# Performance work log

Measured on AMD Instinct MI355X. Metric: run time of the kernel, lower is better.

The kernel has to match this reference:

```python
import jax, jax.numpy as jnp
import numpy as np

N = 150000      # active voxels
C = 64          # head input channels
KK = 9          # 3x3 kernel offsets
H = W = 700     # BEV feature map
BN_EPS = 1e-5
HEADS = [("heatmap", 3), ("center", 2), ("center_z", 1), ("dim", 3), ("rot", 2)]


def _build_neighbor_table(seed=0):
    """Submanifold 3x3 neighbor indices for N active voxels on an HxW grid.
    Entry -1 means the neighbor site is inactive (contributes zero)."""
    rng = np.random.default_rng(seed)
    flat = rng.choice(H * W, size=N, replace=False)
    ys, xs = flat // W, flat % W
    lut = np.full(H * W, -1, np.int64)
    lut[flat] = np.arange(N)
    nbr = np.full((N, KK), -1, np.int64)
    k = 0
    for dy in (-1, 0, 1):
        for dx in (-1, 0, 1):
            ny, nx = ys + dy, xs + dx
            valid = (ny >= 0) & (ny < H) & (nx >= 0) & (nx < W)
            nf = np.where(valid, ny * W + nx, 0)
            nbr[:, k] = np.where(valid, lut[nf], -1)
            k += 1
    return nbr


def setup_inputs() -> dict:
    key = jax.random.key(0)
    ks = jax.random.split(key, 2 + 2 * len(HEADS))
    inp = {
        "features": jax.random.normal(ks[0], (N, C), jnp.float32),
        "nbr_idx": jnp.asarray(_build_neighbor_table(), jnp.int32),
        # one 3x3 subm conv per head, stacked: [n_heads, 9, C_in, C_out]
        "W3": jax.random.normal(ks[1], (len(HEADS), KK, C, C), jnp.float32) * 0.05,
        "gamma": jnp.ones((len(HEADS), C), jnp.float32),
        "beta": jnp.zeros((len(HEADS), C), jnp.float32),
    }
    for i, (name, oc) in enumerate(HEADS):
        inp[f"W1_{name}"] = jax.random.normal(ks[2 + i], (C, oc), jnp.float32) * 0.001
        if name == "heatmap":
            inp[f"b1_{name}"] = jnp.full((oc,), -float(np.log((1 - 0.01) / 0.01)), jnp.float32)
        else:
            inp[f"b1_{name}"] = jnp.zeros((oc,), jnp.float32)
    return inp


def _forward(features, nbr_idx, W3, gamma, beta, W1s, b1s):
    valid = nbr_idx >= 0                                  # [N, 9]
    idx = jnp.where(valid, nbr_idx, 0)
    # gather active-neighbor features; missing neighbors -> zero (subm conv)
    gathered = features[idx] * valid[..., None].astype(features.dtype)  # [N, 9, C]
    # all heads share the same input sparse tensor -> batched gather-GEMM
    h = jnp.einsum('nkc,hkco->hno', gathered, W3)         # [n_heads, N, C]
    # BatchNorm1d (training-mode batch stats, biased var) + ReLU
    mean = h.mean(axis=1, keepdims=True)
    var = ((h - mean) ** 2).mean(axis=1, keepdims=True)
    hn = (h - mean) * jax.lax.rsqrt(var + BN_EPS)
    hn = jax.nn.relu(hn * gamma[:, None, :] + beta[:, None, :])
    # per-head 1x1 subm conv == linear on active features
    return tuple(hn[i] @ W1s[i] + b1s[i] for i in range(len(HEADS)))


def reference(features, nbr_idx, W3, gamma, beta,
              W1_heatmap, b1_heatmap, W1_center, b1_center,
              W1_center_z, b1_center_z, W1_dim, b1_dim, W1_rot, b1_rot):
    W1s = [W1_heatmap, W1_center, W1_center_z, W1_dim, W1_rot]
    b1s = [b1_heatmap, b1_center, b1_center_z, b1_dim, b1_rot]
    return _forward(features, nbr_idx, W3, gamma, beta, W1s, b1s)
```

## Files before the change

kernel.cpp:

```cpp
#include <hip/hip_runtime.h>

#define NVOX 150000
#define BM 128
#define MTILES 1172
#define SROW 150016
#define NCOL 320

typedef __attribute__((ext_vector_type(8))) short bf16x8;
typedef __attribute__((ext_vector_type(4))) float f32x4;

__device__ __forceinline__ unsigned short f2bf(float f) {
    unsigned u = __builtin_bit_cast(unsigned, f);
    u += 0x7fffu + ((u >> 16) & 1u);
    return (unsigned short)(u >> 16);
}

__device__ __forceinline__ void gld16(const void* g, void* l) {
    __builtin_amdgcn_global_load_lds(
        (const __attribute__((address_space(1))) unsigned int*)g,
        (__attribute__((address_space(3))) unsigned int*)l, 16, 0, 0);
}

__global__ void prep_feat(const float* __restrict__ src, unsigned short* __restrict__ dst) {
    int i = blockIdx.x * 256 + threadIdx.x;
    if (i < NVOX * 8) {
        const float* s = src + (size_t)i * 8;
        float4 a = *(const float4*)s;
        float4 b = *(const float4*)(s + 4);
        union { bf16x8 v; unsigned short u[8]; } r;
        r.u[0] = f2bf(a.x); r.u[1] = f2bf(a.y); r.u[2] = f2bf(a.z); r.u[3] = f2bf(a.w);
        r.u[4] = f2bf(b.x); r.u[5] = f2bf(b.y); r.u[6] = f2bf(b.z); r.u[7] = f2bf(b.w);
        *(bf16x8*)(dst + (size_t)i * 8) = r.v;
    } else if (i < NVOX * 8 + 8) {
        bf16x8 z = {0, 0, 0, 0, 0, 0, 0, 0};
        *(bf16x8*)(dst + (size_t)i * 8) = z;
    }
}

__global__ void prep_w3(const float* __restrict__ w3, unsigned short* __restrict__ bt,
                        float* __restrict__ stats) {
    int i = blockIdx.x * 256 + threadIdx.x;
    int h = i / 36864;
    int rem = i - h * 36864;
    int kk = rem >> 12;
    int c = (rem >> 6) & 63;
    int o = rem & 63;
    bt[(size_t)(((h * 9 + kk) * 8) + (c >> 3)) * 512 + o * 8 + (c & 7)] = f2bf(w3[i]);
    if (i < 2 * NCOL) stats[i] = 0.f;
}

__global__ __launch_bounds__(256, 4)
void gemm_kernel(const unsigned short* __restrict__ featB,
                 const unsigned short* __restrict__ Bt2,
                 const int* __restrict__ nbr,
                 unsigned short* __restrict__ hbuf,
                 float* __restrict__ stats) {
    __shared__ __align__(16) char smem[37376];
    constexpr int IDX_OFF = 32768;
    constexpr int SRED_OFF = 32768;

    int bid = blockIdx.x;
    int r = bid & 7, q = bid >> 3;
    int ntile = q % 5;
    int mtile = (q / 5) * 8 + r;
    if (mtile >= MTILES) return;
    int m0 = mtile * BM;
    int n0 = ntile * 64;

    int tid = threadIdx.x;
    int w = tid >> 6, lane = tid & 63;
    int quad = lane >> 4, m16 = lane & 15;

    for (int lin = tid; lin < BM * 9; lin += 256) {
        int row = lin / 9, kkq = lin - row * 9;
        int v = -1;
        if (m0 + row < NVOX) v = nbr[(size_t)(m0 + row) * 9 + kkq];
        *(int*)(smem + IDX_OFF + (kkq * BM + row) * 4) = ((v < 0) ? NVOX : v) * 128;
    }
    __syncthreads();

    f32x4 acc[4][2];
#pragma unroll
    for (int mt = 0; mt < 4; ++mt)
#pragma unroll
        for (int nt = 0; nt < 2; ++nt)
            acc[mt][nt] = (f32x4){0.f, 0.f, 0.f, 0.f};

    const char* fb = (const char*)featB;
    const char* bsrc = (const char*)Bt2 + (size_t)ntile * 73728;
    char* sAb[2] = {smem, smem + 16384};

    int mrow = (w >> 1) * 64;
    int ncol = (w & 1) * 32;
    int c16a = w * 2, c16b = w * 2 + 1;
    const char* bb = bsrc + quad * 1024 + (ncol + m16) * 16;

    bf16x8 bfr[2][2][2];

    auto stageA = [&](char* sA, int off0, int off1) {
        gld16(fb + off0 + c16a * 16, sA + c16a * 2048);
        gld16(fb + off1 + c16a * 16, sA + c16a * 2048 + 1024);
        gld16(fb + off0 + c16b * 16, sA + c16b * 2048);
        gld16(fb + off1 + c16b * 16, sA + c16b * 2048 + 1024);
    };

    {
        int o0 = *(const int*)(smem + IDX_OFF + lane * 4);
        int o1 = *(const int*)(smem + IDX_OFF + (64 + lane) * 4);
        bfr[0][0][0] = *(const bf16x8*)(bb);
        bfr[0][0][1] = *(const bf16x8*)(bb + 256);
        bfr[0][1][0] = *(const bf16x8*)(bb + 4096);
        bfr[0][1][1] = *(const bf16x8*)(bb + 4352);
        stageA(sAb[0], o0, o1);
    }

#pragma unroll
    for (int kk = 0; kk < 9; ++kk) {
        const int p = kk & 1;
        if (kk < 8) {
            int o0 = *(const int*)(smem + IDX_OFF + ((kk + 1) * BM + lane) * 4);
            int o1 = *(const int*)(smem + IDX_OFF + ((kk + 1) * BM + 64 + lane) * 4);
            const char* bk = bb + (size_t)(kk + 1) * 8192;
            bfr[p ^ 1][0][0] = *(const bf16x8*)(bk);
            bfr[p ^ 1][0][1] = *(const bf16x8*)(bk + 256);
            bfr[p ^ 1][1][0] = *(const bf16x8*)(bk + 4096);
            bfr[p ^ 1][1][1] = *(const bf16x8*)(bk + 4352);
            stageA(sAb[p ^ 1], o0, o1);
            asm volatile("s_waitcnt vmcnt(8)" ::: "memory");
        } else {
            asm volatile("s_waitcnt vmcnt(0)" ::: "memory");
        }
        asm volatile("s_barrier" ::: "memory");
        __builtin_amdgcn_sched_barrier(0);
        __builtin_amdgcn_s_setprio(1);
#pragma unroll
        for (int ks = 0; ks < 2; ++ks) {
            bf16x8 af[4];
#pragma unroll
            for (int mt = 0; mt < 4; ++mt)
                af[mt] = *(const bf16x8*)(sAb[p] + (ks * 4 + quad) * 2048 +
                                          (mrow + mt * 16 + m16) * 16);
#pragma unroll
            for (int mt = 0; mt < 4; ++mt)
#pragma unroll
                for (int nt = 0; nt < 2; ++nt)
                    acc[mt][nt] = __builtin_amdgcn_mfma_f32_16x16x32_bf16(
                        af[mt], bfr[p][ks][nt], acc[mt][nt], 0, 0, 0);
        }
        __builtin_amdgcn_s_setprio(0);
        __builtin_amdgcn_sched_barrier(0);
        asm volatile("s_barrier" ::: "memory");
    }

#pragma unroll
    for (int mt = 0; mt < 4; ++mt) {
#pragma unroll
        for (int nt = 0; nt < 2; ++nt) {
            int col = ncol + nt * 16 + m16;
            int row = mrow + mt * 16 + quad * 4;
            f32x4 v = acc[mt][nt];
            unsigned lo = (unsigned)f2bf(v.x) | ((unsigned)f2bf(v.y) << 16);
            unsigned hi = (unsigned)f2bf(v.z) | ((unsigned)f2bf(v.w) << 16);
            uint2 pk; pk.x = lo; pk.y = hi;
            *(uint2*)(smem + col * 272 + row * 2) = pk;
        }
    }
    __syncthreads();
#pragma unroll
    for (int it = 0; it < 8; ++it) {
        int col = it * 8 + (tid >> 5);
        int l32 = tid & 31;
        uint2 v = *(const uint2*)(smem + col * 272 + l32 * 8);
        *(uint2*)(hbuf + (size_t)(n0 + col) * SROW + m0 + l32 * 4) = v;
    }

    float s[2], ss[2];
#pragma unroll
    for (int nt = 0; nt < 2; ++nt) {
        float a = 0.f, b = 0.f;
#pragma unroll
        for (int mt = 0; mt < 4; ++mt) {
            f32x4 v = acc[mt][nt];
            a += v.x + v.y + v.z + v.w;
            b += v.x * v.x + v.y * v.y + v.z * v.z + v.w * v.w;
        }
        s[nt] = a; ss[nt] = b;
        s[nt] += __shfl_xor(s[nt], 16); s[nt] += __shfl_xor(s[nt], 32);
        ss[nt] += __shfl_xor(ss[nt], 16); ss[nt] += __shfl_xor(ss[nt], 32);
    }
    if (quad == 0) {
#pragma unroll
        for (int nt = 0; nt < 2; ++nt) {
            float* p = (float*)(smem + SRED_OFF + ((w * 2 + nt) * 16 + m16) * 8);
            p[0] = s[nt]; p[1] = ss[nt];
        }
    }
    __syncthreads();
    if (tid < 64) {
        int col = tid;
        int half = col >> 5, nt = (col >> 4) & 1, mc = col & 15;
        const float* p0 = (const float*)(smem + SRED_OFF + ((half * 2 + nt) * 16 + mc) * 8);
        const float* p1 = (const float*)(smem + SRED_OFF + (((2 + half) * 2 + nt) * 16 + mc) * 8);
        atomicAdd(&stats[n0 + col], p0[0] + p1[0]);
        atomicAdd(&stats[NCOL + n0 + col], p0[1] + p1[1]);
    }
}

__global__ __launch_bounds__(256)
void head_kernel(const unsigned short* __restrict__ hbuf,
                 const float* __restrict__ stats,
                 const float* __restrict__ gamma, const float* __restrict__ beta,
                 const float* __restrict__ W1_0, const float* __restrict__ W1_1,
                 const float* __restrict__ W1_2, const float* __restrict__ W1_3,
                 const float* __restrict__ W1_4,
                 const float* __restrict__ b1_0, const float* __restrict__ b1_1,
                 const float* __restrict__ b1_2, const float* __restrict__ b1_3,
                 const float* __restrict__ b1_4,
                 float* __restrict__ out) {
    __shared__ float sScale[64], sShift[64], sW1[192], sB1[3];
    int h = blockIdx.y;
    const float* W1; const float* b1; int oc; size_t obase;
    if (h == 0)      { W1 = W1_0; b1 = b1_0; oc = 3; obase = 0; }
    else if (h == 1) { W1 = W1_1; b1 = b1_1; oc = 2; obase = 450000; }
    else if (h == 2) { W1 = W1_2; b1 = b1_2; oc = 1; obase = 750000; }
    else if (h == 3) { W1 = W1_3; b1 = b1_3; oc = 3; obase = 900000; }
    else             { W1 = W1_4; b1 = b1_4; oc = 2; obase = 1350000; }

    int tid = threadIdx.x;
    if (tid < 64) {
        int c = h * 64 + tid;
        float mean = stats[c] * (1.f / (float)NVOX);
        float var = stats[NCOL + c] * (1.f / (float)NVOX) - mean * mean;
        float inv = rsqrtf(var + 1e-5f);
        float sc = inv * gamma[c];
        sScale[tid] = sc;
        sShift[tid] = beta[c] - mean * sc;
    }
    for (int i = tid; i < 192; i += 256) {
        int cc = i / 3, jj = i - cc * 3;
        sW1[i] = (jj < oc) ? W1[cc * oc + jj] : 0.f;
    }
    if (tid == 0) {
        sB1[0] = b1[0];
        sB1[1] = (oc >= 2) ? b1[1] : 0.f;
        sB1[2] = (oc >= 3) ? b1[2] : 0.f;
    }
    __syncthreads();

    int n = (blockIdx.x * 256 + tid) * 4;
    if (n >= NVOX) return;
    const unsigned short* hp = hbuf + (size_t)(h * 64) * SROW + n;
    float x[4][3];
#pragma unroll
    for (int rr = 0; rr < 4; ++rr) { x[rr][0] = sB1[0]; x[rr][1] = sB1[1]; x[rr][2] = sB1[2]; }
#pragma unroll 8
    for (int cc = 0; cc < 64; ++cc) {
        uint2 raw = *(const uint2*)(hp + (size_t)cc * SROW);
        float sc = sScale[cc], sh = sShift[cc];
        float w0 = sW1[cc * 3 + 0], w1 = sW1[cc * 3 + 1], w2 = sW1[cc * 3 + 2];
        float v0 = __builtin_bit_cast(float, raw.x << 16);
        float v1 = __builtin_bit_cast(float, raw.x & 0xffff0000u);
        float v2 = __builtin_bit_cast(float, raw.y << 16);
        float v3 = __builtin_bit_cast(float, raw.y & 0xffff0000u);
        v0 = fmaxf(v0 * sc + sh, 0.f); v1 = fmaxf(v1 * sc + sh, 0.f);
        v2 = fmaxf(v2 * sc + sh, 0.f); v3 = fmaxf(v3 * sc + sh, 0.f);
        x[0][0] += v0 * w0; x[0][1] += v0 * w1; x[0][2] += v0 * w2;
        x[1][0] += v1 * w0; x[1][1] += v1 * w1; x[1][2] += v1 * w2;
        x[2][0] += v2 * w0; x[2][1] += v2 * w1; x[2][2] += v2 * w2;
        x[3][0] += v3 * w0; x[3][1] += v3 * w1; x[3][2] += v3 * w2;
    }
#pragma unroll
    for (int rr = 0; rr < 4; ++rr) {
        float* op = out + obase + (size_t)(n + rr) * oc;
        op[0] = x[rr][0];
        if (oc >= 2) op[1] = x[rr][1];
        if (oc >= 3) op[2] = x[rr][2];
    }
}

extern "C" void kernel_launch(void* const* d_in, const int* in_sizes, int n_in,
                              void* d_out, int out_size, void* d_ws, size_t ws_size,
                              hipStream_t stream) {
    const float* features = (const float*)d_in[0];
    const int* nbr        = (const int*)d_in[1];
    const float* w3       = (const float*)d_in[2];
    const float* gamma    = (const float*)d_in[3];
    const float* beta     = (const float*)d_in[4];
    const float* W1_0 = (const float*)d_in[5];  const float* b1_0 = (const float*)d_in[6];
    const float* W1_1 = (const float*)d_in[7];  const float* b1_1 = (const float*)d_in[8];
    const float* W1_2 = (const float*)d_in[9];  const float* b1_2 = (const float*)d_in[10];
    const float* W1_3 = (const float*)d_in[11]; const float* b1_3 = (const float*)d_in[12];
    const float* W1_4 = (const float*)d_in[13]; const float* b1_4 = (const float*)d_in[14];
    float* out = (float*)d_out;

    char* ws = (char*)d_ws;
    unsigned short* featB = (unsigned short*)ws;
    unsigned short* Bt2   = (unsigned short*)(ws + 19200128);
    float* stats          = (float*)(ws + 19568768);
    unsigned short* hbuf  = (unsigned short*)(ws + 19571328);

    prep_feat<<<(NVOX * 8 + 8 + 255) / 256, 256, 0, stream>>>(features, featB);
    prep_w3<<<184320 / 256, 256, 0, stream>>>(w3, Bt2, stats);
    gemm_kernel<<<8 * 5 * 147, 256, 0, stream>>>(featB, Bt2, nbr, hbuf, stats);
    head_kernel<<<dim3(147, 5), 256, 0, stream>>>(hbuf, stats, gamma, beta,
        W1_0, W1_1, W1_2, W1_3, W1_4, b1_0, b1_1, b1_2, b1_3, b1_4, out);
}
```

Measured before the change: 223.7 us.

## Compute all 320 output columns per block to gather features once

The gather-GEMM is restructured so that each 512-thread block handles one 128-row M tile across all five heads (320 columns), instead of five separate 64-column blocks. Each gathered feature row is then fetched once rather than five times. Weights are now staged through LDS with async loads instead of being held in registers. In exchange the kernel uses about 116KB of LDS and 20 accumulators per wave, which lowers occupancy to roughly one block per CU, and there are fewer blocks (1172).

```diff
diff --git a/kernel.cpp b/kernel.cpp
--- a/kernel.cpp
+++ b/kernel.cpp
@@ -49,29 +49,25 @@
     if (i < 2 * NCOL) stats[i] = 0.f;
 }
 
-__global__ __launch_bounds__(256, 4)
+__global__ __launch_bounds__(512, 2)
 void gemm_kernel(const unsigned short* __restrict__ featB,
                  const unsigned short* __restrict__ Bt2,
                  const int* __restrict__ nbr,
                  unsigned short* __restrict__ hbuf,
                  float* __restrict__ stats) {
-    __shared__ __align__(16) char smem[37376];
-    constexpr int IDX_OFF = 32768;
-    constexpr int SRED_OFF = 32768;
-
-    int bid = blockIdx.x;
-    int r = bid & 7, q = bid >> 3;
-    int ntile = q % 5;
-    int mtile = (q / 5) * 8 + r;
-    if (mtile >= MTILES) return;
+    __shared__ __align__(16) char smem[119296];
+    constexpr int SB_OFF = 32768;
+    constexpr int IDX_OFF = 114688;
+    constexpr int SRED_OFF = 88064;
+
+    int mtile = blockIdx.x;
     int m0 = mtile * BM;
-    int n0 = ntile * 64;
 
     int tid = threadIdx.x;
     int w = tid >> 6, lane = tid & 63;
     int quad = lane >> 4, m16 = lane & 15;
 
-    for (int lin = tid; lin < BM * 9; lin += 256) {
+    for (int lin = tid; lin < BM * 9; lin += 512) {
         int row = lin / 9, kkq = lin - row * 9;
         int v = -1;
         if (m0 + row < NVOX) v = nbr[(size_t)(m0 + row) * 9 + kkq];
@@ -79,54 +75,57 @@
     }
     __syncthreads();
 
-    f32x4 acc[4][2];
+    f32x4 acc[4][5];
 #pragma unroll
     for (int mt = 0; mt < 4; ++mt)
 #pragma unroll
-        for (int nt = 0; nt < 2; ++nt)
+        for (int nt = 0; nt < 5; ++nt)
             acc[mt][nt] = (f32x4){0.f, 0.f, 0.f, 0.f};
 
     const char* fb = (const char*)featB;
-    const char* bsrc = (const char*)Bt2 + (size_t)ntile * 73728;
+    const char* bt = (const char*)Bt2;
     char* sAb[2] = {smem, smem + 16384};
-
-    int mrow = (w >> 1) * 64;
-    int ncol = (w & 1) * 32;
-    int c16a = w * 2, c16b = w * 2 + 1;
-    const char* bb = bsrc + quad * 1024 + (ncol + m16) * 16;
-
-    bf16x8 bfr[2][2][2];
-
-    auto stageA = [&](char* sA, int off0, int off1) {
-        gld16(fb + off0 + c16a * 16, sA + c16a * 2048);
-        gld16(fb + off1 + c16a * 16, sA + c16a * 2048 + 1024);
-        gld16(fb + off0 + c16b * 16, sA + c16b * 2048);
-        gld16(fb + off1 + c16b * 16, sA + c16b * 2048 + 1024);
+    char* sBb[2] = {smem + SB_OFF, smem + SB_OFF + 40960};
+
+    int mrow = (w >> 2) * 64;
+    int half = w >> 2;
+    int cbase = (w & 3) * 80;
+
+    int bsj[5], bdj[5];
+#pragma unroll
+    for (int j = 0; j < 5; ++j) {
+        int u = w * 5 + j;
+        int h = u >> 3, c16 = u & 7;
+        bsj[j] = (h * 72 + c16) * 1024 + lane * 16;
+        bdj[j] = (h * 8 + c16) * 1024;
+    }
+    int sBoff[5];
+#pragma unroll
+    for (int nt = 0; nt < 5; ++nt) {
+        int c = cbase + nt * 16 + m16;
+        sBoff[nt] = (c >> 6) * 8192 + (c & 63) * 16;
+    }
+
+    auto stage = [&](int buf, int kk) {
+        int off0 = *(const int*)(smem + IDX_OFF + (kk * BM + lane) * 4);
+        int off1 = *(const int*)(smem + IDX_OFF + (kk * BM + 64 + lane) * 4);
+        char* sA = sAb[buf];
+        char* sB = sBb[buf];
+        gld16(fb + off0 + w * 16, sA + w * 2048);
+        gld16(fb + off1 + w * 16, sA + w * 2048 + 1024);
+#pragma unroll
+        for (int j = 0; j < 5; ++j)
+            gld16(bt + (size_t)(bsj[j] + kk * 8192), sB + bdj[j]);
     };
 
-    {
-        int o0 = *(const int*)(smem + IDX_OFF + lane * 4);
-        int o1 = *(const int*)(smem + IDX_OFF + (64 + lane) * 4);
-        bfr[0][0][0] = *(const bf16x8*)(bb);
-        bfr[0][0][1] = *(const bf16x8*)(bb + 256);
-        bfr[0][1][0] = *(const bf16x8*)(bb + 4096);
-        bfr[0][1][1] = *(const bf16x8*)(bb + 4352);
-        stageA(sAb[0], o0, o1);
-    }
+    stage(0, 0);
 
 #pragma unroll
     for (int kk = 0; kk < 9; ++kk) {
         const int p = kk & 1;
         if (kk < 8) {
-            int o0 = *(const int*)(smem + IDX_OFF + ((kk + 1) * BM + lane) * 4);
-            int o1 = *(const int*)(smem + IDX_OFF + ((kk + 1) * BM + 64 + lane) * 4);
-            const char* bk = bb + (size_t)(kk + 1) * 8192;
-            bfr[p ^ 1][0][0] = *(const bf16x8*)(bk);
-            bfr[p ^ 1][0][1] = *(const bf16x8*)(bk + 256);
-            bfr[p ^ 1][1][0] = *(const bf16x8*)(bk + 4096);
-            bfr[p ^ 1][1][1] = *(const bf16x8*)(bk + 4352);
-            stageA(sAb[p ^ 1], o0, o1);
-            asm volatile("s_waitcnt vmcnt(8)" ::: "memory");
+            stage(p ^ 1, kk + 1);
+            asm volatile("s_waitcnt vmcnt(7)" ::: "memory");
         } else {
             asm volatile("s_waitcnt vmcnt(0)" ::: "memory");
         }
@@ -135,17 +134,20 @@
         __builtin_amdgcn_s_setprio(1);
 #pragma unroll
         for (int ks = 0; ks < 2; ++ks) {
-            bf16x8 af[4];
+            bf16x8 af[4], bf[5];
 #pragma unroll
             for (int mt = 0; mt < 4; ++mt)
                 af[mt] = *(const bf16x8*)(sAb[p] + (ks * 4 + quad) * 2048 +
-                                          (mrow + mt * 16 + m16) * 16);
+                                          half * 1024 + (mt * 16 + m16) * 16);
+#pragma unroll
+            for (int nt = 0; nt < 5; ++nt)
+                bf[nt] = *(const bf16x8*)(sBb[p] + sBoff[nt] + (ks * 4 + quad) * 1024);
 #pragma unroll
             for (int mt = 0; mt < 4; ++mt)
 #pragma unroll
-                for (int nt = 0; nt < 2; ++nt)
+                for (int nt = 0; nt < 5; ++nt)
                     acc[mt][nt] = __builtin_amdgcn_mfma_f32_16x16x32_bf16(
-                        af[mt], bfr[p][ks][nt], acc[mt][nt], 0, 0, 0);
+                        af[mt], bf[nt], acc[mt][nt], 0, 0, 0);
         }
         __builtin_amdgcn_s_setprio(0);
         __builtin_amdgcn_sched_barrier(0);
@@ -155,8 +157,8 @@
 #pragma unroll
     for (int mt = 0; mt < 4; ++mt) {
 #pragma unroll
-        for (int nt = 0; nt < 2; ++nt) {
-            int col = ncol + nt * 16 + m16;
+        for (int nt = 0; nt < 5; ++nt) {
+            int col = cbase + nt * 16 + m16;
             int row = mrow + mt * 16 + quad * 4;
             f32x4 v = acc[mt][nt];
             unsigned lo = (unsigned)f2bf(v.x) | ((unsigned)f2bf(v.y) << 16);
@@ -167,16 +169,16 @@
     }
     __syncthreads();
 #pragma unroll
-    for (int it = 0; it < 8; ++it) {
-        int col = it * 8 + (tid >> 5);
+    for (int it = 0; it < 20; ++it) {
+        int col = it * 16 + (tid >> 5);
         int l32 = tid & 31;
         uint2 v = *(const uint2*)(smem + col * 272 + l32 * 8);
-        *(uint2*)(hbuf + (size_t)(n0 + col) * SROW + m0 + l32 * 4) = v;
-    }
-
-    float s[2], ss[2];
-#pragma unroll
-    for (int nt = 0; nt < 2; ++nt) {
+        *(uint2*)(hbuf + (size_t)col * SROW + m0 + l32 * 4) = v;
+    }
+
+    float s[5], ss[5];
+#pragma unroll
+    for (int nt = 0; nt < 5; ++nt) {
         float a = 0.f, b = 0.f;
 #pragma unroll
         for (int mt = 0; mt < 4; ++mt) {
@@ -190,19 +192,19 @@
     }
     if (quad == 0) {
 #pragma unroll
-        for (int nt = 0; nt < 2; ++nt) {
-            float* p = (float*)(smem + SRED_OFF + ((w * 2 + nt) * 16 + m16) * 8);
+        for (int nt = 0; nt < 5; ++nt) {
+            float* p = (float*)(smem + SRED_OFF + (w * 80 + nt * 16 + m16) * 8);
             p[0] = s[nt]; p[1] = ss[nt];
         }
     }
     __syncthreads();
-    if (tid < 64) {
-        int col = tid;
-        int half = col >> 5, nt = (col >> 4) & 1, mc = col & 15;
-        const float* p0 = (const float*)(smem + SRED_OFF + ((half * 2 + nt) * 16 + mc) * 8);
-        const float* p1 = (const float*)(smem + SRED_OFF + (((2 + half) * 2 + nt) * 16 + mc) * 8);
-        atomicAdd(&stats[n0 + col], p0[0] + p1[0]);
-        atomicAdd(&stats[NCOL + n0 + col], p0[1] + p1[1]);
+    if (tid < NCOL) {
+        int c = tid;
+        int qq = c / 80, lc = c - qq * 80;
+        const float* p0 = (const float*)(smem + SRED_OFF + (qq * 80 + lc) * 8);
+        const float* p1 = (const float*)(smem + SRED_OFF + ((qq + 4) * 80 + lc) * 8);
+        atomicAdd(&stats[c], p0[0] + p1[0]);
+        atomicAdd(&stats[NCOL + c], p0[1] + p1[1]);
     }
 }
 
@@ -301,7 +303,7 @@
 
     prep_feat<<<(NVOX * 8 + 8 + 255) / 256, 256, 0, stream>>>(features, featB);
     prep_w3<<<184320 / 256, 256, 0, stream>>>(w3, Bt2, stats);
-    gemm_kernel<<<8 * 5 * 147, 256, 0, stream>>>(featB, Bt2, nbr, hbuf, stats);
+    gemm_kernel<<<MTILES, 512, 0, stream>>>(featB, Bt2, nbr, hbuf, stats);
     head_kernel<<<dim3(147, 5), 256, 0, stream>>>(hbuf, stats, gamma, beta,
         W1_0, W1_1, W1_2, W1_3, W1_4, b1_0, b1_1, b1_2, b1_3, b1_4, out);
 }
```

New measurement: 219.3 us. 2.0% less time.
